# Kernel optimization log

Measured on AMD Instinct MI355X. Metric: run time of the kernel, lower is better.

Reference implementation:

```python
import jax, jax.numpy as jnp
import numpy as np

EPS = 1e-5

def conv1d(x, w, b, pad):
    # x: [N, Cin, T], w: [Cout, Cin, K]
    y = jax.lax.conv_general_dilated(x, w, (1,), [(pad, pad)],
                                     dimension_numbers=("NCH", "OIH", "NCH"))
    return y + b[None, :, None]

def bn_eval(x, gamma, beta, mean, var):
    # BatchNorm1d in inference mode over channel dim of [N, C, T]
    inv = gamma / jnp.sqrt(var + EPS)
    return x * inv[None, :, None] + (beta - mean * inv)[None, :, None]

def setup_inputs() -> dict:
    key = jax.random.key(0)
    ks = jax.random.split(key, 16)
    B, E, N, T = 8, 16, 64, 128
    D, OUT = 32, 64  # timeseries_dim, output_dim
    inp = {
        "node_features": jax.random.normal(ks[0], (B, E, N, T, 1), dtype=jnp.float32),
        "edge_features": jax.random.normal(ks[1], (B, E, T), dtype=jnp.float32),
        "conv1_w": jax.random.normal(ks[2], (D, 1, 3), dtype=jnp.float32) * 0.3,
        "conv1_b": jax.random.normal(ks[3], (D,), dtype=jnp.float32) * 0.1,
        "conv2_w": jax.random.normal(ks[4], (1, D, 3), dtype=jnp.float32) * 0.1,
        "conv2_b": jax.random.normal(ks[5], (1,), dtype=jnp.float32) * 0.1,
        "conv3_w": jax.random.normal(ks[6], (OUT, 1, 1), dtype=jnp.float32) * 0.3,
        "conv3_b": jax.random.normal(ks[7], (OUT,), dtype=jnp.float32) * 0.1,
        "bn1_gamma": jax.random.uniform(ks[8], (D,), dtype=jnp.float32) + 0.5,
        "bn1_beta": jax.random.normal(ks[9], (D,), dtype=jnp.float32) * 0.1,
        "bn1_mean": jax.random.normal(ks[10], (D,), dtype=jnp.float32) * 0.1,
        "bn1_var": jax.random.uniform(ks[11], (D,), dtype=jnp.float32) + 0.5,
        "bn2_gamma": jax.random.uniform(ks[12], (1,), dtype=jnp.float32) + 0.5,
        "bn2_beta": jax.random.normal(ks[13], (1,), dtype=jnp.float32) * 0.1,
        "bn2_mean": jax.random.normal(ks[14], (1,), dtype=jnp.float32) * 0.1,
        "bn2_var": jax.random.uniform(ks[15], (1,), dtype=jnp.float32) + 0.5,
    }
    return inp

def reference(node_features, edge_features, conv1_w, conv1_b, conv2_w, conv2_b,
              conv3_w, conv3_b, bn1_gamma, bn1_beta, bn1_mean, bn1_var,
              bn2_gamma, bn2_beta, bn2_mean, bn2_var):
    B, E, N, T, _ = node_features.shape
    OUT = conv3_w.shape[0]
    # Self-connectivity: each (b,e,n) node processes its own [1,1,T] series and
    # the sum over its (single) connected edge is the identity. Fuse the triple
    # python loop into one batched conv pipeline over B*E*N series.
    x = node_features.reshape(B * E * N, 1, T)          # [BEN, 1, T]
    x = jax.nn.relu(bn_eval(conv1d(x, conv1_w, conv1_b, 1),
                            bn1_gamma, bn1_beta, bn1_mean, bn1_var))  # [BEN, D, T]
    x = jax.nn.relu(bn_eval(conv1d(x, conv2_w, conv2_b, 1),
                            bn2_gamma, bn2_beta, bn2_mean, bn2_var))  # [BEN, 1, T]
    x = conv1d(x, conv3_w, conv3_b, 0)                  # [BEN, OUT, T]
    return x.reshape(B, E, N, OUT, T)
```

## Files before the change

### kernel.cpp

```cpp
#include <hip/hip_runtime.h>

#define EPSF 1e-5f
#define SER 4

typedef float f32x4 __attribute__((ext_vector_type(4)));


__global__ __launch_bounds__(128) void hnc_kernel(
    const float* __restrict__ x_in,
    const float* __restrict__ w1,
    const float* __restrict__ b1,
    const float* __restrict__ w2,
    const float* __restrict__ b2,
    const float* __restrict__ w3,
    const float* __restrict__ b3,
    const float* __restrict__ g1, const float* __restrict__ be1,
    const float* __restrict__ m1, const float* __restrict__ v1,
    const float* __restrict__ g2, const float* __restrict__ be2,
    const float* __restrict__ m2, const float* __restrict__ v2,
    float* __restrict__ out)
{
    __shared__ float x_s[SER][132];
    __shared__ f32x4 pkA_s[32];
    __shared__ f32x4 pkB_s[32];
    __shared__ float w3_s[64];
    __shared__ float b3_s[64];
    __shared__ float c2_s;

    const int tid  = threadIdx.x;
    const int lane = tid & 63;
    const size_t s0 = (size_t)blockIdx.x * SER;

    #pragma unroll
    for (int s = 0; s < SER; ++s)
        x_s[s][2 + tid] = x_in[(s0 + s) * 128 + tid];
    if (tid < SER) {
        x_s[tid][0] = 0.f; x_s[tid][1] = 0.f;
        x_s[tid][130] = 0.f; x_s[tid][131] = 0.f;
    }
    if (tid < 32) {
        const int d = tid;
        float inv = g1[d] * rsqrtf(v1[d] + EPSF);
        f32x4 A;
        A.x = inv * w1[d * 3 + 0];
        A.y = inv * w1[d * 3 + 1];
        A.z = inv * w1[d * 3 + 2];
        A.w = b1[d] * inv + be1[d] - m1[d] * inv;
        pkA_s[d] = A;
    } else if (tid < 64) {
        const int d = tid - 32;
        float s2 = g2[0] * rsqrtf(v2[0] + EPSF);
        f32x4 W;
        W.x = s2 * w2[d * 3 + 0];
        W.y = s2 * w2[d * 3 + 1];
        W.z = s2 * w2[d * 3 + 2];
        W.w = 0.f;
        pkB_s[d] = W;
        if (d == 0) c2_s = b2[0] * s2 + be2[0] - m2[0] * s2;
    } else {
        const int o = tid - 64;
        w3_s[o] = w3[o];
        b3_s[o] = b3[o];
    }
    __syncthreads();

    const int g  = lane >> 4;
    const int qq = (tid >> 6) * 16 + (lane & 15);
    const int srcl = 4 * (lane & 15);
    float w3r[16], b3r[16];
    #pragma unroll
    for (int i = 0; i < 16; ++i) {
        w3r[i] = w3_s[4 * i + g];
        b3r[i] = b3_s[4 * i + g];
    }
    const float mm = (tid == 0)   ? 0.f : 1.f;
    const float mp = (tid == 127) ? 0.f : 1.f;
    const float c2 = c2_s;

    for (int s = 0; s < SER; ++s) {
        const float xm2 = x_s[s][tid];
        const float xm1 = x_s[s][tid + 1];
        const float x0  = x_s[s][tid + 2];
        const float xp1 = x_s[s][tid + 3];
        const float xp2 = x_s[s][tid + 4];

        float accm = 0.f, acc0 = 0.f, accp = 0.f;
        #pragma unroll 4
        for (int d = 0; d < 32; ++d) {
            const f32x4 A = pkA_s[d];
            const f32x4 W = pkB_s[d];
            float ym = fmaxf(fmaf(A.x, xm2, fmaf(A.y, xm1, fmaf(A.z, x0,  A.w))), 0.f);
            float y0 = fmaxf(fmaf(A.x, xm1, fmaf(A.y, x0,  fmaf(A.z, xp1, A.w))), 0.f);
            float yp = fmaxf(fmaf(A.x, x0,  fmaf(A.y, xp1, fmaf(A.z, xp2, A.w))), 0.f);
            accm = fmaf(W.x, ym, accm);
            acc0 = fmaf(W.y, y0, acc0);
            accp = fmaf(W.z, yp, accp);
        }
        const float y2v = fmaxf(fmaf(mm, accm, fmaf(mp, accp, acc0 + c2)), 0.f);

        f32x4 y;
        y.x = __shfl(y2v, srcl + 0, 64);
        y.y = __shfl(y2v, srcl + 1, 64);
        y.z = __shfl(y2v, srcl + 2, 64);
        y.w = __shfl(y2v, srcl + 3, 64);

        f32x4* out4 = (f32x4*)(out + (s0 + s) * 64 * 128);
        #pragma unroll
        for (int i = 0; i < 16; ++i) {
            f32x4 r;
            r.x = fmaf(w3r[i], y.x, b3r[i]);
            r.y = fmaf(w3r[i], y.y, b3r[i]);
            r.z = fmaf(w3r[i], y.z, b3r[i]);
            r.w = fmaf(w3r[i], y.w, b3r[i]);
            out4[(4 * i + g) * 32 + qq] = r;
        }
    }
}

extern "C" void kernel_launch(void* const* d_in, const int* in_sizes, int n_in,
                              void* d_out, int out_size, void* d_ws, size_t ws_size,
                              hipStream_t stream) {
    const float* x   = (const float*)d_in[0];
    const float* w1  = (const float*)d_in[2];
    const float* b1  = (const float*)d_in[3];
    const float* w2  = (const float*)d_in[4];
    const float* b2  = (const float*)d_in[5];
    const float* w3  = (const float*)d_in[6];
    const float* b3  = (const float*)d_in[7];
    const float* g1  = (const float*)d_in[8];
    const float* be1 = (const float*)d_in[9];
    const float* m1  = (const float*)d_in[10];
    const float* v1  = (const float*)d_in[11];
    const float* g2  = (const float*)d_in[12];
    const float* be2 = (const float*)d_in[13];
    const float* m2  = (const float*)d_in[14];
    const float* v2  = (const float*)d_in[15];

    const int T = 128;
    const int n_series = in_sizes[0] / T;
    const int n_blocks = n_series / SER;

    hnc_kernel<<<n_blocks, 128, 0, stream>>>(x, w1, b1, w2, b2, w3, b3,
                                             g1, be1, m1, v1, g2, be2, m2, v2,
                                             (float*)d_out);
}
```

Before: 49.55 us.

## Split fused pipeline into compute kernel and grid-strided output expansion kernel

The single fused kernel is split in two. The first computes the conv1/bn/conv2 result per series and writes it to a workspace buffer. The second is a grid-strided kernel with 2048 blocks of 256 threads that reads those values back and writes the 64-channel conv3 output as float4 stores. The intent is to separate the compute-bound stage from the write-bandwidth-bound expansion so the large output write runs at full occupancy and stays coalesced. The cost is an extra launch plus a workspace round trip, and the iteration count assumes the total output divides evenly by the grid size.

After: 71.21 us. 1.44x slower.

```diff
diff --git a/kernel.cpp b/kernel.cpp
--- a/kernel.cpp
+++ b/kernel.cpp
@@ -6,29 +6,22 @@
 typedef float f32x4 __attribute__((ext_vector_type(4)));
 
 
-__global__ __launch_bounds__(128) void hnc_kernel(
+__global__ __launch_bounds__(128) void y2_kernel(
     const float* __restrict__ x_in,
-    const float* __restrict__ w1,
-    const float* __restrict__ b1,
-    const float* __restrict__ w2,
-    const float* __restrict__ b2,
-    const float* __restrict__ w3,
-    const float* __restrict__ b3,
+    const float* __restrict__ w1, const float* __restrict__ b1,
+    const float* __restrict__ w2, const float* __restrict__ b2,
     const float* __restrict__ g1, const float* __restrict__ be1,
     const float* __restrict__ m1, const float* __restrict__ v1,
     const float* __restrict__ g2, const float* __restrict__ be2,
     const float* __restrict__ m2, const float* __restrict__ v2,
-    float* __restrict__ out)
+    float* __restrict__ y2ws)
 {
     __shared__ float x_s[SER][132];
     __shared__ f32x4 pkA_s[32];
     __shared__ f32x4 pkB_s[32];
-    __shared__ float w3_s[64];
-    __shared__ float b3_s[64];
     __shared__ float c2_s;
 
-    const int tid  = threadIdx.x;
-    const int lane = tid & 63;
+    const int tid = threadIdx.x;
     const size_t s0 = (size_t)blockIdx.x * SER;
 
     #pragma unroll
@@ -57,26 +50,14 @@
         W.w = 0.f;
         pkB_s[d] = W;
         if (d == 0) c2_s = b2[0] * s2 + be2[0] - m2[0] * s2;
-    } else {
-        const int o = tid - 64;
-        w3_s[o] = w3[o];
-        b3_s[o] = b3[o];
     }
     __syncthreads();
 
-    const int g  = lane >> 4;
-    const int qq = (tid >> 6) * 16 + (lane & 15);
-    const int srcl = 4 * (lane & 15);
-    float w3r[16], b3r[16];
-    #pragma unroll
-    for (int i = 0; i < 16; ++i) {
-        w3r[i] = w3_s[4 * i + g];
-        b3r[i] = b3_s[4 * i + g];
-    }
     const float mm = (tid == 0)   ? 0.f : 1.f;
     const float mp = (tid == 127) ? 0.f : 1.f;
     const float c2 = c2_s;
 
+    #pragma unroll
     for (int s = 0; s < SER; ++s) {
         const float xm2 = x_s[s][tid];
         const float xm1 = x_s[s][tid + 1];
@@ -96,24 +77,38 @@
             acc0 = fmaf(W.y, y0, acc0);
             accp = fmaf(W.z, yp, accp);
         }
-        const float y2v = fmaxf(fmaf(mm, accm, fmaf(mp, accp, acc0 + c2)), 0.f);
+        y2ws[(s0 + s) * 128 + tid] =
+            fmaxf(fmaf(mm, accm, fmaf(mp, accp, acc0 + c2)), 0.f);
+    }
+}
 
-        f32x4 y;
-        y.x = __shfl(y2v, srcl + 0, 64);
-        y.y = __shfl(y2v, srcl + 1, 64);
-        y.z = __shfl(y2v, srcl + 2, 64);
-        y.w = __shfl(y2v, srcl + 3, 64);
+__global__ __launch_bounds__(256) void expand_kernel(
+    const float* __restrict__ y2ws,
+    const float* __restrict__ w3,
+    const float* __restrict__ b3,
+    float* __restrict__ out,
+    int n_iters)
+{
+    const int f0 = blockIdx.x * 256 + threadIdx.x;
+    const int o  = (f0 >> 5) & 63;
+    const int q  = f0 & 31;
+    const float w = w3[o];
+    const float b = b3[o];
+    const int stride = gridDim.x * 256;
+    const int s_step = stride >> 11;
 
-        f32x4* out4 = (f32x4*)(out + (s0 + s) * 64 * 128);
-        #pragma unroll
-        for (int i = 0; i < 16; ++i) {
-            f32x4 r;
-            r.x = fmaf(w3r[i], y.x, b3r[i]);
-            r.y = fmaf(w3r[i], y.y, b3r[i]);
-            r.z = fmaf(w3r[i], y.z, b3r[i]);
-            r.w = fmaf(w3r[i], y.w, b3r[i]);
-            out4[(4 * i + g) * 32 + qq] = r;
-        }
+    const f32x4* ysrc = (const f32x4*)(y2ws + (size_t)(f0 >> 11) * 128) + q;
+    f32x4* dst = (f32x4*)out + f0;
+
+    #pragma unroll 4
+    for (int it = 0; it < n_iters; ++it) {
+        const f32x4 y = ysrc[(size_t)it * s_step * 32];
+        f32x4 r;
+        r.x = fmaf(w, y.x, b);
+        r.y = fmaf(w, y.y, b);
+        r.z = fmaf(w, y.z, b);
+        r.w = fmaf(w, y.w, b);
+        dst[(size_t)it * stride] = r;
     }
 }
 
@@ -138,9 +133,14 @@
 
     const int T = 128;
     const int n_series = in_sizes[0] / T;
-    const int n_blocks = n_series / SER;
+    float* y2ws = (float*)d_ws;
 
-    hnc_kernel<<<n_blocks, 128, 0, stream>>>(x, w1, b1, w2, b2, w3, b3,
-                                             g1, be1, m1, v1, g2, be2, m2, v2,
-                                             (float*)d_out);
+    y2_kernel<<<n_series / SER, 128, 0, stream>>>(
+        x, w1, b1, w2, b2, g1, be1, m1, v1, g2, be2, m2, v2, y2ws);
+
+    const int n_quads  = n_series * 64 * 128 / 4;
+    const int n_blocks = 2048;
+    const int n_iters  = n_quads / (n_blocks * 256);
+    expand_kernel<<<n_blocks, 256, 0, stream>>>(y2ws, w3, b3, (float*)d_out,
+                                                n_iters);
 }
```
